# Kernel tuning notes

Measured on AMD Instinct MI355X. Metric: run time of the kernel, lower is better.

## Reference

```python
import jax, jax.numpy as jnp
import numpy as np

NUM_CATEGORIES = 32
INPUT_DIM = 1536
HIDDEN_DIM = 1024
OUTPUT_DIM = 1024
B, T = 128, 32


def setup_inputs() -> dict:
    key = jax.random.key(0)
    k_x, k_cat, k_w1, k_w2 = jax.random.split(key, 4)
    x = jax.random.normal(k_x, (B, T, INPUT_DIM), dtype=jnp.float32)
    cat_ids = jax.random.randint(k_cat, (B,), 0, NUM_CATEGORIES)
    # CategorySpecificLinear params: W ~ 0.02*randn, b = zeros
    W1 = 0.02 * jax.random.normal(k_w1, (NUM_CATEGORIES, INPUT_DIM, HIDDEN_DIM), dtype=jnp.float32)
    b1 = jnp.zeros((NUM_CATEGORIES, HIDDEN_DIM), dtype=jnp.float32)
    W2 = 0.02 * jax.random.normal(k_w2, (NUM_CATEGORIES, HIDDEN_DIM, OUTPUT_DIM), dtype=jnp.float32)
    b2 = jnp.zeros((NUM_CATEGORIES, OUTPUT_DIM), dtype=jnp.float32)
    return {"x": x, "cat_ids": cat_ids, "W1": W1, "b1": b1, "W2": W2, "b2": b2}


def _cat_linear(x, W, b, cat_ids):
    # x: (B, T, D_in); W: (C, D_in, D_out); b: (C, D_out)
    # torch: bmm(x, W[cat_ids]) + b[cat_ids].unsqueeze(1)
    return jnp.einsum("btd,bdh->bth", x, W[cat_ids]) + b[cat_ids][:, None, :]


def reference(x, cat_ids, W1, b1, W2, b2):
    # CategorySpecificMLP.forward
    hidden = jax.nn.relu(_cat_linear(x, W1, b1, cat_ids))  # (B, T, H)
    return _cat_linear(hidden, W2, b2, cat_ids)            # (B, T, O)
```

## Files before the change

kernel.cpp:

```cpp
#include <hip/hip_runtime.h>
#include <hip/hip_bf16.h>
#include <stdint.h>

#define NCAT 32
#define DIN  1536
#define DMID 1024
#define NB   128
#define TT   32

#define BM 128
#define BN 64
#define BK 32
#define LDA 40
#define MAXG 56

typedef __attribute__((ext_vector_type(8))) short short8;
typedef __attribute__((ext_vector_type(4))) float f32x4;

static __device__ __forceinline__ unsigned int pk2bf(float lo, float hi) {
  unsigned short a = __builtin_bit_cast(unsigned short, __float2bfloat16(lo));
  unsigned short b = __builtin_bit_cast(unsigned short, __float2bfloat16(hi));
  return ((unsigned int)b << 16) | (unsigned int)a;
}

__global__ void build_groups(const int* __restrict__ cat_ids, int* __restrict__ wsi) {
  __shared__ int cats[NB];
  __shared__ int cnt[NCAT];
  __shared__ int off[NCAT];
  int t = threadIdx.x;
  cats[t] = cat_ids[t];
  __syncthreads();
  if (t < NCAT) {
    int n = 0;
    for (int b = 0; b < NB; b++) n += (cats[b] == t);
    cnt[t] = n;
  }
  __syncthreads();
  if (t == 0) {
    int acc = 0;
    for (int c = 0; c < NCAT; c++) { off[c] = acc; acc += cnt[c]; }
  }
  __syncthreads();
  if (t < NCAT) {
    int o = off[t];
    for (int b = 0; b < NB; b++)
      if (cats[b] == t) wsi[o++] = b;
  }
  if (t == 0) {
    int g = 0;
    for (int c = 0; c < NCAT; c++) {
      int n = cnt[c], o = off[c];
      for (int j = 0; j < n; j += 4) {
        wsi[132 + g * 4 + 0] = c;
        wsi[132 + g * 4 + 1] = o + j;
        wsi[132 + g * 4 + 2] = (n - j) < 4 ? (n - j) : 4;
        g++;
      }
    }
    wsi[128] = g;
  }
}

template <int LAYER>
__global__ __launch_bounds__(256)
void mlp_gemm(const void* __restrict__ Ain, const float* __restrict__ W,
              const float* __restrict__ bias, const int* __restrict__ wsi,
              void* __restrict__ Out, int K) {
  int gid = blockIdx.y;
  if (gid >= wsi[128]) return;
  const int cat   = wsi[132 + gid * 4 + 0];
  const int start = wsi[132 + gid * 4 + 1];
  const int cnt   = wsi[132 + gid * 4 + 2];
  const int n0    = blockIdx.x * BN;

  __shared__ unsigned short As[BM * LDA];
  __shared__ unsigned short Bs[4 * BN * 8];

  const int tid  = threadIdx.x;
  const int lane = tid & 63;
  const int w    = tid >> 6;

  const int arow  = tid >> 1;
  const int khalf = (tid & 1) * 16;
  const int lb    = arow >> 5;
  const int tok   = arow & 31;
  const int lbc   = lb < (cnt - 1) ? lb : (cnt - 1);
  const int batch = wsi[start + lbc];
  const long grow = (long)(batch * TT + tok);

  const float* Wcol = W + (size_t)cat * (size_t)K * 1024 + n0 + lane;

  f32x4 acc[4][2];
#pragma unroll
  for (int i = 0; i < 4; i++)
#pragma unroll
    for (int j = 0; j < 2; j++) acc[i][j] = (f32x4){0.f, 0.f, 0.f, 0.f};

  const int wm  = (w >> 1) * 64;
  const int wn  = (w & 1) * 32;
  const int kg  = lane >> 4;
  const int c16 = lane & 15;

  auto load_tile = [&](int k0, float4 ar[4], uint4& ah0, uint4& ah1, float br[8]) {
    if constexpr (LAYER == 1) {
      const float* ap = (const float*)Ain + grow * (long)K + k0 + khalf;
      ar[0] = *(const float4*)(ap + 0);
      ar[1] = *(const float4*)(ap + 4);
      ar[2] = *(const float4*)(ap + 8);
      ar[3] = *(const float4*)(ap + 12);
    } else {
      const uint4* ap = (const uint4*)((const unsigned short*)Ain + grow * (long)K + k0 + khalf);
      ah0 = ap[0];
      ah1 = ap[1];
    }
    const float* bp = Wcol + (size_t)(k0 + w * 8) * 1024;
#pragma unroll
    for (int r = 0; r < 8; r++) br[r] = bp[(size_t)r * 1024];
  };

  auto store_tile = [&](const float4 ar[4], const uint4& ah0, const uint4& ah1,
                        const float br[8]) {
    if constexpr (LAYER == 1) {
      uint4 aw0 = make_uint4(pk2bf(ar[0].x, ar[0].y), pk2bf(ar[0].z, ar[0].w),
                             pk2bf(ar[1].x, ar[1].y), pk2bf(ar[1].z, ar[1].w));
      uint4 aw1 = make_uint4(pk2bf(ar[2].x, ar[2].y), pk2bf(ar[2].z, ar[2].w),
                             pk2bf(ar[3].x, ar[3].y), pk2bf(ar[3].z, ar[3].w));
      *(uint4*)&As[arow * LDA + khalf]     = aw0;
      *(uint4*)&As[arow * LDA + khalf + 8] = aw1;
    } else {
      *(uint4*)&As[arow * LDA + khalf]     = ah0;
      *(uint4*)&As[arow * LDA + khalf + 8] = ah1;
    }
    uint4 bw = make_uint4(pk2bf(br[0], br[1]), pk2bf(br[2], br[3]),
                          pk2bf(br[4], br[5]), pk2bf(br[6], br[7]));
    *(uint4*)&Bs[(w * BN + lane) * 8] = bw;
  };

  float4 arC[4]; uint4 ah0C, ah1C; float brC[8];
  load_tile(0, arC, ah0C, ah1C, brC);

  for (int k0 = 0; k0 < K; k0 += BK) {
    __syncthreads();
    store_tile(arC, ah0C, ah1C, brC);
    __syncthreads();

    float4 arN[4]; uint4 ah0N, ah1N; float brN[8];
    if (k0 + BK < K) load_tile(k0 + BK, arN, ah0N, ah1N, brN);

    short8 afrag[4], bfrag[2];
#pragma unroll
    for (int i = 0; i < 4; i++)
      afrag[i] = *(const short8*)&As[(wm + i * 16 + c16) * LDA + kg * 8];
#pragma unroll
    for (int j = 0; j < 2; j++)
      bfrag[j] = *(const short8*)&Bs[(kg * BN + wn + j * 16 + c16) * 8];
#pragma unroll
    for (int i = 0; i < 4; i++)
#pragma unroll
      for (int j = 0; j < 2; j++)
        acc[i][j] = __builtin_amdgcn_mfma_f32_16x16x32_bf16(afrag[i], bfrag[j], acc[i][j], 0, 0, 0);

#pragma unroll
    for (int i = 0; i < 4; i++) arC[i] = arN[i];
    ah0C = ah0N; ah1C = ah1N;
#pragma unroll
    for (int r = 0; r < 8; r++) brC[r] = brN[r];
  }

  const int rquad = (lane >> 4) * 4;
#pragma unroll
  for (int i = 0; i < 4; i++) {
#pragma unroll
    for (int j = 0; j < 2; j++) {
      int gcol = n0 + wn + j * 16 + c16;
      float bb = bias[cat * 1024 + gcol];
#pragma unroll
      for (int r = 0; r < 4; r++) {
        int lrow = wm + i * 16 + rquad + r;
        int lb2 = lrow >> 5;
        if (lb2 < cnt) {
          int b2 = wsi[start + lb2];
          long orow = (long)(b2 * TT + (lrow & 31));
          float v = acc[i][j][r] + bb;
          if constexpr (LAYER == 1) {
            v = fmaxf(v, 0.f);
            ((unsigned short*)Out)[orow * DMID + gcol] =
                __builtin_bit_cast(unsigned short, __float2bfloat16(v));
          } else {
            ((float*)Out)[orow * 1024 + gcol] = v;
          }
        }
      }
    }
  }
}

extern "C" void kernel_launch(void* const* d_in, const int* in_sizes, int n_in,
                              void* d_out, int out_size, void* d_ws, size_t ws_size,
                              hipStream_t stream) {
  const float* x       = (const float*)d_in[0];
  const int*   cat_ids = (const int*)d_in[1];
  const float* W1      = (const float*)d_in[2];
  const float* b1      = (const float*)d_in[3];
  const float* W2      = (const float*)d_in[4];
  const float* b2      = (const float*)d_in[5];
  float* out = (float*)d_out;

  int* wsi = (int*)d_ws;
  unsigned short* hidden = (unsigned short*)((char*)d_ws + 8192);

  build_groups<<<dim3(1), dim3(128), 0, stream>>>(cat_ids, wsi);
  mlp_gemm<1><<<dim3(1024 / BN, MAXG), dim3(256), 0, stream>>>(
      (const void*)x, W1, b1, wsi, (void*)hidden, DIN);
  mlp_gemm<2><<<dim3(1024 / BN, MAXG), dim3(256), 0, stream>>>(
      (const void*)hidden, W2, b2, wsi, (void*)out, DMID);
}
```

Before: 444.8 us.

## Pre-convert x to bf16, double-buffer LDS tiles, and remap blocks for L2 locality

Adds a separate kernel that converts x to bf16 once, so layer-1 GEMM blocks load bf16 activations instead of converting fp32 per tile, and each x row is not re-converted by all 16 column tiles. Shared-memory A/B tiles are double-buffered, which drops one barrier per K step and lets the next tile's store overlap the current MFMAs. The grid becomes 1-D with a swizzled mapping that groups 8 groups across the column tiles, meant to improve W and A reuse in cache. This costs an extra kernel launch and 12 MB of extra workspace traffic, and doubles LDS use per block.

```diff
diff --git a/kernel.cpp b/kernel.cpp
--- a/kernel.cpp
+++ b/kernel.cpp
@@ -13,6 +13,7 @@
 #define BK 32
 #define LDA 40
 #define MAXG 56
+#define NTILE 16
 
 typedef __attribute__((ext_vector_type(8))) short short8;
 typedef __attribute__((ext_vector_type(4))) float f32x4;
@@ -61,20 +62,30 @@
   }
 }
 
+__global__ void cvt_x_bf16(const float* __restrict__ in, unsigned short* __restrict__ out) {
+  int i = blockIdx.x * 256 + threadIdx.x;
+  const float4* p = (const float4*)in + (size_t)i * 2;
+  float4 a = p[0], b = p[1];
+  ((uint4*)out)[i] = make_uint4(pk2bf(a.x, a.y), pk2bf(a.z, a.w),
+                                pk2bf(b.x, b.y), pk2bf(b.z, b.w));
+}
+
 template <int LAYER>
 __global__ __launch_bounds__(256)
-void mlp_gemm(const void* __restrict__ Ain, const float* __restrict__ W,
+void mlp_gemm(const unsigned short* __restrict__ A, const float* __restrict__ W,
               const float* __restrict__ bias, const int* __restrict__ wsi,
               void* __restrict__ Out, int K) {
-  int gid = blockIdx.y;
-  if (gid >= wsi[128]) return;
-  const int cat   = wsi[132 + gid * 4 + 0];
-  const int start = wsi[132 + gid * 4 + 1];
-  const int cnt   = wsi[132 + gid * 4 + 2];
-  const int n0    = blockIdx.x * BN;
-
-  __shared__ unsigned short As[BM * LDA];
-  __shared__ unsigned short Bs[4 * BN * 8];
+  const int id = blockIdx.x;
+  const int g  = (id & 7) + 8 * (id >> 7);
+  const int t  = (id >> 3) & 15;
+  if (g >= wsi[128]) return;
+  const int cat   = wsi[132 + g * 4 + 0];
+  const int start = wsi[132 + g * 4 + 1];
+  const int cnt   = wsi[132 + g * 4 + 2];
+  const int n0    = t * BN;
+
+  __shared__ unsigned short As[2][BM * LDA];
+  __shared__ unsigned short Bs[2][4 * BN * 8];
 
   const int tid  = threadIdx.x;
   const int lane = tid & 63;
@@ -87,6 +98,7 @@
   const int lbc   = lb < (cnt - 1) ? lb : (cnt - 1);
   const int batch = wsi[start + lbc];
   const long grow = (long)(batch * TT + tok);
+  const unsigned short* Arow = A + grow * (long)K + khalf;
 
   const float* Wcol = W + (size_t)cat * (size_t)K * 1024 + n0 + lane;
 
@@ -101,70 +113,48 @@
   const int kg  = lane >> 4;
   const int c16 = lane & 15;
 
-  auto load_tile = [&](int k0, float4 ar[4], uint4& ah0, uint4& ah1, float br[8]) {
-    if constexpr (LAYER == 1) {
-      const float* ap = (const float*)Ain + grow * (long)K + k0 + khalf;
-      ar[0] = *(const float4*)(ap + 0);
-      ar[1] = *(const float4*)(ap + 4);
-      ar[2] = *(const float4*)(ap + 8);
-      ar[3] = *(const float4*)(ap + 12);
-    } else {
-      const uint4* ap = (const uint4*)((const unsigned short*)Ain + grow * (long)K + k0 + khalf);
-      ah0 = ap[0];
-      ah1 = ap[1];
-    }
+  uint4 a0, a1;
+  float br[8];
+  auto load_tile = [&](int k0) {
+    const uint4* ap = (const uint4*)(Arow + k0);
+    a0 = ap[0];
+    a1 = ap[1];
     const float* bp = Wcol + (size_t)(k0 + w * 8) * 1024;
 #pragma unroll
     for (int r = 0; r < 8; r++) br[r] = bp[(size_t)r * 1024];
   };
-
-  auto store_tile = [&](const float4 ar[4], const uint4& ah0, const uint4& ah1,
-                        const float br[8]) {
-    if constexpr (LAYER == 1) {
-      uint4 aw0 = make_uint4(pk2bf(ar[0].x, ar[0].y), pk2bf(ar[0].z, ar[0].w),
-                             pk2bf(ar[1].x, ar[1].y), pk2bf(ar[1].z, ar[1].w));
-      uint4 aw1 = make_uint4(pk2bf(ar[2].x, ar[2].y), pk2bf(ar[2].z, ar[2].w),
-                             pk2bf(ar[3].x, ar[3].y), pk2bf(ar[3].z, ar[3].w));
-      *(uint4*)&As[arow * LDA + khalf]     = aw0;
-      *(uint4*)&As[arow * LDA + khalf + 8] = aw1;
-    } else {
-      *(uint4*)&As[arow * LDA + khalf]     = ah0;
-      *(uint4*)&As[arow * LDA + khalf + 8] = ah1;
-    }
+  auto store_tile = [&](int buf) {
+    *(uint4*)&As[buf][arow * LDA + khalf]     = a0;
+    *(uint4*)&As[buf][arow * LDA + khalf + 8] = a1;
     uint4 bw = make_uint4(pk2bf(br[0], br[1]), pk2bf(br[2], br[3]),
                           pk2bf(br[4], br[5]), pk2bf(br[6], br[7]));
-    *(uint4*)&Bs[(w * BN + lane) * 8] = bw;
+    *(uint4*)&Bs[buf][(w * BN + lane) * 8] = bw;
   };
 
-  float4 arC[4]; uint4 ah0C, ah1C; float brC[8];
-  load_tile(0, arC, ah0C, ah1C, brC);
+  load_tile(0);
+  store_tile(0);
+  int cur = 0;
 
   for (int k0 = 0; k0 < K; k0 += BK) {
     __syncthreads();
-    store_tile(arC, ah0C, ah1C, brC);
-    __syncthreads();
-
-    float4 arN[4]; uint4 ah0N, ah1N; float brN[8];
-    if (k0 + BK < K) load_tile(k0 + BK, arN, ah0N, ah1N, brN);
+    const bool more = (k0 + BK) < K;
+    if (more) load_tile(k0 + BK);
 
     short8 afrag[4], bfrag[2];
 #pragma unroll
     for (int i = 0; i < 4; i++)
-      afrag[i] = *(const short8*)&As[(wm + i * 16 + c16) * LDA + kg * 8];
+      afrag[i] = *(const short8*)&As[cur][(wm + i * 16 + c16) * LDA + kg * 8];
 #pragma unroll
     for (int j = 0; j < 2; j++)
-      bfrag[j] = *(const short8*)&Bs[(kg * BN + wn + j * 16 + c16) * 8];
+      bfrag[j] = *(const short8*)&Bs[cur][(kg * BN + wn + j * 16 + c16) * 8];
 #pragma unroll
     for (int i = 0; i < 4; i++)
 #pragma unroll
       for (int j = 0; j < 2; j++)
         acc[i][j] = __builtin_amdgcn_mfma_f32_16x16x32_bf16(afrag[i], bfrag[j], acc[i][j], 0, 0, 0);
 
-#pragma unroll
-    for (int i = 0; i < 4; i++) arC[i] = arN[i];
-    ah0C = ah0N; ah1C = ah1N;
-#pragma unroll
-    for (int r = 0; r < 8; r++) brC[r] = brN[r];
+    if (more) store_tile(cur ^ 1);
+    cur ^= 1;
   }
 
   const int rquad = (lane >> 4) * 4;
@@ -207,11 +197,13 @@
   float* out = (float*)d_out;
 
   int* wsi = (int*)d_ws;
-  unsigned short* hidden = (unsigned short*)((char*)d_ws + 8192);
+  unsigned short* xbf    = (unsigned short*)((char*)d_ws + 8192);
+  unsigned short* hidden = (unsigned short*)((char*)d_ws + 8192 + 12582912);
 
   build_groups<<<dim3(1), dim3(128), 0, stream>>>(cat_ids, wsi);
-  mlp_gemm<1><<<dim3(1024 / BN, MAXG), dim3(256), 0, stream>>>(
-      (const void*)x, W1, b1, wsi, (void*)hidden, DIN);
-  mlp_gemm<2><<<dim3(1024 / BN, MAXG), dim3(256), 0, stream>>>(
-      (const void*)hidden, W2, b2, wsi, (void*)out, DMID);
-}
+  cvt_x_bf16<<<dim3(3072), dim3(256), 0, stream>>>(x, xbf);
+  mlp_gemm<1><<<dim3(NTILE * MAXG), dim3(256), 0, stream>>>(
+      xbf, W1, b1, wsi, (void*)hidden, DIN);
+  mlp_gemm<2><<<dim3(NTILE * MAXG), dim3(256), 0, stream>>>(
+      hidden, W2, b2, wsi, (void*)out, DMID);
+}
```

Result: no change. 446.7 us (+0.4%).
